# Performance work log

Measured on AMD Instinct MI355X. Metric: run time of the kernel, lower is better.

The kernel has to match this reference:

```python
import jax, jax.numpy as jnp
import numpy as np

NEG = -1e10

def setup_inputs() -> dict:
    key = jax.random.key(0)
    ks = jax.random.split(key, 7)
    B, Q, K = 8, 128, 512
    d_q, d_kv, d_attn = 512, 512, 256
    query = jax.random.normal(ks[0], (B, Q, d_q), dtype=jnp.float32)
    kv = jax.random.normal(ks[1], (B, K, d_kv), dtype=jnp.float32)
    query_len = jax.random.randint(ks[2], (B,), 1, Q + 1)
    kv_len = jax.random.randint(ks[3], (B,), 1, K + 1)
    # h2attn: Linear(d_q+d_kv, d_attn) -> weight [d_attn, d_q+d_kv], bias [d_attn]
    W = jax.random.normal(ks[4], (d_attn, d_q + d_kv), dtype=jnp.float32) / np.sqrt(d_q + d_kv)
    b = jnp.zeros((d_attn,), dtype=jnp.float32)
    v = jax.random.normal(ks[5], (d_attn,), dtype=jnp.float32)
    return {"query": query, "kv": kv, "W": W, "b": b, "v": v,
            "query_len": query_len, "kv_len": kv_len}

def reference(query, kv, W, b, v, query_len, kv_len):
    B, Q, d_q = query.shape
    _, K, d_kv = kv.shape
    # Split the concat-linear: W @ [q; kv] == Wq @ q + Wk @ kv (same math, no huge concat)
    Wq, Wk = W[:, :d_q], W[:, d_q:]
    q_proj = jnp.einsum('bqd,ad->bqa', query, Wq)   # [B,Q,d_attn]
    k_proj = jnp.einsum('bkd,ad->bka', kv, Wk)      # [B,K,d_attn]
    e = jnp.tanh(q_proj[:, :, None, :] + k_proj[:, None, :, :] + b)  # [B,Q,K,d_attn]
    score = jnp.einsum('bqka,a->bqk', e, v)          # [B,Q,K]
    mask_q = jnp.arange(Q)[None, :] < query_len[:, None]   # [B,Q]
    mask_k = jnp.arange(K)[None, :] < kv_len[:, None]      # [B,K]
    score = jnp.where(mask_q[:, :, None], score, NEG)
    score = jnp.where(mask_k[:, None, :], score, NEG)
    attn = jax.nn.softmax(score, axis=-1)
    out = jnp.einsum('bqk,bkd->bqd', attn, kv)       # [B,Q,d_kv]
    return out
```

## Files before the change

### kernel.cpp

```cpp
#include <hip/hip_runtime.h>

#define NEGV (-10000000000.0f)

typedef unsigned short u16;
typedef _Float16 __attribute__((ext_vector_type(8))) f16x8;
typedef _Float16 __attribute__((ext_vector_type(4))) f16x4;
typedef __attribute__((ext_vector_type(4))) float f32x4;

__device__ __forceinline__ u16 f2fh(float f) {
  _Float16 h = (_Float16)f;
  return __builtin_bit_cast(u16, h);
}

__device__ __forceinline__ void gload16(const u16* g, u16* l) {
  __builtin_amdgcn_global_load_lds(
      (const __attribute__((address_space(1))) void*)g,
      (__attribute__((address_space(3))) void*)l, 16, 0, 0);
}

__device__ __forceinline__ f16x8 cvt8(float4 x, float4 y) {
  f16x8 o;
  o[0] = (_Float16)x.x; o[1] = (_Float16)x.y;
  o[2] = (_Float16)x.z; o[3] = (_Float16)x.w;
  o[4] = (_Float16)y.x; o[5] = (_Float16)y.y;
  o[6] = (_Float16)y.z; o[7] = (_Float16)y.w;
  return o;
}

__device__ __forceinline__ void mfma_tile(const u16* sA, const u16* sB,
                                          int l, int wr, int wc,
                                          f32x4 (*acc)[2]) {
#pragma unroll
  for (int ks = 0; ks < 2; ks++) {
    f16x8 af[2], bfr[2];
#pragma unroll
    for (int f = 0; f < 2; f++) {
      int cb = (ks * 32 + ((l >> 4) << 3)) << 1;
      int row = wr * 32 + f * 16 + (l & 15);
      af[f] = *(const f16x8*)((const char*)sA + row * 128 + (cb ^ ((row & 7) << 4)));
      int col = wc * 32 + f * 16 + (l & 15);
      bfr[f] = *(const f16x8*)((const char*)sB + col * 128 + (cb ^ ((col & 7) << 4)));
    }
#pragma unroll
    for (int fm = 0; fm < 2; fm++)
#pragma unroll
      for (int fn = 0; fn < 2; fn++)
        acc[fm][fn] = __builtin_amdgcn_mfma_f32_16x16x32_f16(
            af[fm], bfr[fn], acc[fm][fn], 0, 0, 0);
  }
}

__global__ __launch_bounds__(256) void proj_mfma(
    const float* __restrict__ query, const float* __restrict__ kv,
    const float* __restrict__ W, const float* __restrict__ bias,
    const int* __restrict__ qlen_p, const int* __restrict__ klen_p,
    float* __restrict__ qpE, float* __restrict__ kpE)
{
  const int p = blockIdx.x;
  const int id = (p & 7) * 40 + (p >> 3);
  const int t = threadIdx.x;

  const float *A, *B; float* C;
  int lda, ldb, ldc, bm, bn;
  const float* bp = nullptr;
  if (id < 64) {
    bm = (id >> 2) * 64; bn = (id & 3) * 64;
    if ((bm & 127) >= qlen_p[bm >> 7]) return;
    A = query; lda = 512; B = W; ldb = 1024;
    C = qpE; ldc = 256;
    bp = bias;
  } else {
    int r = id - 64;
    int b = r >> 5, w5 = r & 31;
    bm = (w5 & 3) * 64; bn = (w5 >> 2) * 64;
    if (bn >= klen_p[b]) return;
    A = W + 512; lda = 1024;
    B = kv + (size_t)b * 512 * 512; ldb = 512;
    C = kpE + (size_t)b * 256 * 512; ldc = 512;
  }

  __shared__ __align__(16) u16 sA[8 * 512];
  __shared__ __align__(16) u16 sB[8 * 512];

  const int l = t & 63, w = t >> 6;
  const int wr = w >> 1, wc = w & 1;
  const int r0 = t >> 3, oc = t & 7;
  const int sw0 = (oc * 16) ^ ((r0 & 7) << 4);

  f32x4 acc[2][2] = {};
  float4 a00, a01, a10, a11, b00, b01, b10, b11;

  auto LOAD = [&](int k0) {
    const float* pa0 = A + (size_t)(bm + r0) * lda + k0 + oc * 8;
    const float* pa1 = pa0 + (size_t)32 * lda;
    a00 = *(const float4*)pa0; a01 = *(const float4*)(pa0 + 4);
    a10 = *(const float4*)pa1; a11 = *(const float4*)(pa1 + 4);
    const float* pb0 = B + (size_t)(bn + r0) * ldb + k0 + oc * 8;
    const float* pb1 = pb0 + (size_t)32 * ldb;
    b00 = *(const float4*)pb0; b01 = *(const float4*)(pb0 + 4);
    b10 = *(const float4*)pb1; b11 = *(const float4*)(pb1 + 4);
  };
  auto WRITE = [&]() {
    *(f16x8*)((char*)sA + r0 * 128 + sw0)        = cvt8(a00, a01);
    *(f16x8*)((char*)sA + (r0 + 32) * 128 + sw0) = cvt8(a10, a11);
    *(f16x8*)((char*)sB + r0 * 128 + sw0)        = cvt8(b00, b01);
    *(f16x8*)((char*)sB + (r0 + 32) * 128 + sw0) = cvt8(b10, b11);
  };

  LOAD(0);
  for (int k0 = 0; k0 < 512; k0 += 64) {
    __syncthreads();
    WRITE();
    if (k0 + 64 < 512) LOAD(k0 + 64);
    __syncthreads();
    mfma_tile(sA, sB, l, wr, wc, acc);
  }

#pragma unroll
  for (int fm = 0; fm < 2; fm++)
#pragma unroll
    for (int fn = 0; fn < 2; fn++) {
      int cn = bn + wc * 32 + fn * 16 + (l & 15);
      float bv = bp ? bp[cn] : 0.0f;
#pragma unroll
      for (int j = 0; j < 4; j++) {
        int rm = bm + wr * 32 + fm * 16 + (l >> 4) * 4 + j;
        C[(size_t)rm * ldc + cn] = __expf((acc[fm][fn][j] + bv) * 2.0f);
      }
    }
}

__global__ __launch_bounds__(512) void score_softmax(
    const float* __restrict__ qpE,
    const float* __restrict__ kpE,
    const float* __restrict__ v,
    const int* __restrict__ qlen_p, const int* __restrict__ klen_p,
    u16* __restrict__ P)
{
  const int p = blockIdx.x;
  const int log = (p & 7) * 32 + (p >> 3);
  const int b = log >> 5, q0 = (log & 31) * 4;
  const int t = threadIdx.x;
  const int qlen = qlen_p[b], klen = klen_p[b];
  const int w = t >> 6, l = t & 63;
  const int k = t;
  u16* Pb = P + (size_t)(b * 128 + q0) * 512;

  if (q0 >= qlen) {
    const u16 uh = f2fh(1.0f / 512.0f);
#pragma unroll
    for (int r = 0; r < 4; r++) Pb[(size_t)r * 512 + k] = uh;
    return;
  }

  __shared__ float sEq[256][4];
  __shared__ float sV2[256];
  __shared__ float sRed[8][8];

  {
    int a = t & 255, rr = t >> 8;
    sEq[a][rr]     = qpE[(size_t)(b * 128 + q0 + rr) * 256 + a];
    sEq[a][rr + 2] = qpE[(size_t)(b * 128 + q0 + rr + 2) * 256 + a];
    if (t < 256) sV2[t] = 2.0f * v[t];
  }
  __syncthreads();

  float s[4] = {0.f, 0.f, 0.f, 0.f};
  if (w * 64 < klen) {
    const float* kc = kpE + (size_t)b * 256 * 512 + k;
#pragma unroll 8
    for (int a = 0; a < 256; a++) {
      float ek = kc[(size_t)a * 512];
      f32x4 eq = *(const f32x4*)&sEq[a][0];
      float vv = sV2[a];
#pragma unroll
      for (int r = 0; r < 4; r++)
        s[r] = fmaf(-vv, __builtin_amdgcn_rcpf(fmaf(eq[r], ek, 1.0f)), s[r]);
    }
  }
  if (k >= klen) {
#pragma unroll
    for (int r = 0; r < 4; r++) s[r] = NEGV;
  }

#pragma unroll
  for (int r = 0; r < 4; r++) {
    float x = s[r];
#pragma unroll
    for (int off = 32; off > 0; off >>= 1) x = fmaxf(x, __shfl_xor(x, off));
    if (l == 0) sRed[w][r] = x;
  }
  __syncthreads();
  float e[4];
#pragma unroll
  for (int r = 0; r < 4; r++) {
    float mm = fmaxf(fmaxf(sRed[0][r], sRed[1][r]),
                     fmaxf(sRed[2][r], sRed[3][r]));
    mm = fmaxf(mm, fmaxf(fmaxf(sRed[4][r], sRed[5][r]),
                         fmaxf(sRed[6][r], sRed[7][r])));
    e[r] = __expf(s[r] - mm);
  }
  __syncthreads();
#pragma unroll
  for (int r = 0; r < 4; r++) {
    float x = e[r];
#pragma unroll
    for (int off = 32; off > 0; off >>= 1) x += __shfl_xor(x, off);
    if (l == 0) sRed[w][4 + r] = x;
  }
  __syncthreads();

  const u16 uh = f2fh(1.0f / 512.0f);
#pragma unroll
  for (int r = 0; r < 4; r++) {
    float S = (sRed[0][4 + r] + sRed[1][4 + r]) +
              (sRed[2][4 + r] + sRed[3][4 + r]) +
              (sRed[4][4 + r] + sRed[5][4 + r]) +
              (sRed[6][4 + r] + sRed[7][4 + r]);
    float pp = e[r] * __fdividef(1.0f, S);
    Pb[(size_t)r * 512 + k] = (q0 + r < qlen) ? f2fh(pp) : uh;
  }
}

__global__ __launch_bounds__(256) void pv_mfma(
    const u16* __restrict__ P, const float* __restrict__ kv,
    float* __restrict__ out)
{
  __shared__ __align__(16) u16 sA[8 * 512];
  __shared__ __align__(16) u16 sB[8 * 512];
  const int p = blockIdx.x;
  const int log = (p & 7) * 16 + (p >> 3);
  const int t = threadIdx.x;
  const int b = log >> 4, r = log & 15;
  const int bm = (r >> 3) * 64, bn = (r & 7) * 64;

  const u16* Ab = P + (size_t)b * 128 * 512;
  const float* Bb = kv + (size_t)b * 512 * 512;

  const int l = t & 63, w = t >> 6;
  const int wr = w >> 1, wc = w & 1;
  const int srow = l >> 3, scol = ((l & 7) ^ srow) << 3;

  const int dq = t & 15, kq = t >> 4;

  float4 v0, v1, v2, v3;
  auto LOADB = [&](int k0) {
    const float* pp = Bb + (size_t)(k0 + kq * 4) * 512 + bn + dq * 4;
    v0 = *(const float4*)pp;
    v1 = *(const float4*)(pp + 512);
    v2 = *(const float4*)(pp + 1024);
    v3 = *(const float4*)(pp + 1536);
  };
  auto WRITEB = [&]() {
#define WRB(jj, ee)                                                       \
    { int d = dq * 4 + jj;                                                \
      f16x4 c; c[0] = (_Float16)v0.ee; c[1] = (_Float16)v1.ee;            \
      c[2] = (_Float16)v2.ee; c[3] = (_Float16)v3.ee;                     \
      *(f16x4*)((char*)sB + d * 128 +                                     \
                ((((kq >> 1) * 16) ^ ((d & 7) << 4)) + (kq & 1) * 8)) = c; }
    WRB(0, x) WRB(1, y) WRB(2, z) WRB(3, w)
#undef WRB
  };

  f32x4 acc[2][2] = {};
  LOADB(0);
  for (int k0 = 0; k0 < 512; k0 += 64) {
    __syncthreads();
    WRITEB();
#pragma unroll
    for (int i = 0; i < 2; i++) {
      int s = w * 2 + i;
      gload16(Ab + (size_t)(bm + s * 8 + srow) * 512 + k0 + scol, sA + s * 512);
    }
    if (k0 + 64 < 512) LOADB(k0 + 64);
    __syncthreads();
    mfma_tile(sA, sB, l, wr, wc, acc);
  }

  float* Cb = out + (size_t)b * 128 * 512;
#pragma unroll
  for (int fm = 0; fm < 2; fm++)
#pragma unroll
    for (int fn = 0; fn < 2; fn++) {
      int cn = bn + wc * 32 + fn * 16 + (l & 15);
#pragma unroll
      for (int j = 0; j < 4; j++) {
        int rm = bm + wr * 32 + fm * 16 + (l >> 4) * 4 + j;
        Cb[(size_t)rm * 512 + cn] = acc[fm][fn][j];
      }
    }
}

extern "C" void kernel_launch(void* const* d_in, const int* in_sizes, int n_in,
                              void* d_out, int out_size, void* d_ws, size_t ws_size,
                              hipStream_t stream)
{
  const float* query = (const float*)d_in[0];
  const float* kv    = (const float*)d_in[1];
  const float* W     = (const float*)d_in[2];
  const float* bbias = (const float*)d_in[3];
  const float* v     = (const float*)d_in[4];
  const int*   qlen  = (const int*)d_in[5];
  const int*   klen  = (const int*)d_in[6];
  float* out = (float*)d_out;

  float* qpE = (float*)d_ws;
  float* kpE = qpE + 1024 * 256;
  u16*   P   = (u16*)(kpE + 8 * 256 * 512);

  proj_mfma<<<dim3(320), 256, 0, stream>>>(
      query, kv, W, bbias, qlen, klen, qpE, kpE);

  score_softmax<<<dim3(256), 512, 0, stream>>>(
      qpE, kpE, v, qlen, klen, P);

  pv_mfma<<<dim3(128), 256, 0, stream>>>(P, kv, out);
}
```

Baseline: 40.40 us.

## Use 128x128 tiles for key projection and skip masked K blocks in PV

The key-projection part of proj_mfma now uses 128x128 output tiles with 4x4 MFMA fragments per wave, which cuts the block count from 320 to 128 and increases operand reuse per block. The query projection keeps its 64x64 tiles. In pv_mfma, row blocks whose query rows are all valid loop only up to the padded kv_len, since softmax probabilities past kv_len are zero. The trade-off is fewer, heavier blocks with more registers in the projection, and possibly poorer load balance.

```diff
diff --git a/kernel.cpp b/kernel.cpp
--- a/kernel.cpp
+++ b/kernel.cpp
@@ -50,84 +50,152 @@
   }
 }
 
+__device__ __forceinline__ void mfma_tile128(const u16* sA, const u16* sB,
+                                             int l, int wr, int wc,
+                                             f32x4 (*acc)[4]) {
+#pragma unroll
+  for (int ks = 0; ks < 2; ks++) {
+    f16x8 af[4], bfr[4];
+#pragma unroll
+    for (int f = 0; f < 4; f++) {
+      int cb = (ks * 32 + ((l >> 4) << 3)) << 1;
+      int row = wr * 64 + f * 16 + (l & 15);
+      af[f] = *(const f16x8*)((const char*)sA + row * 128 + (cb ^ ((row & 7) << 4)));
+      int col = wc * 64 + f * 16 + (l & 15);
+      bfr[f] = *(const f16x8*)((const char*)sB + col * 128 + (cb ^ ((col & 7) << 4)));
+    }
+#pragma unroll
+    for (int fm = 0; fm < 4; fm++)
+#pragma unroll
+      for (int fn = 0; fn < 4; fn++)
+        acc[fm][fn] = __builtin_amdgcn_mfma_f32_16x16x32_f16(
+            af[fm], bfr[fn], acc[fm][fn], 0, 0, 0);
+  }
+}
+
 __global__ __launch_bounds__(256) void proj_mfma(
     const float* __restrict__ query, const float* __restrict__ kv,
     const float* __restrict__ W, const float* __restrict__ bias,
     const int* __restrict__ qlen_p, const int* __restrict__ klen_p,
     float* __restrict__ qpE, float* __restrict__ kpE)
 {
+  __shared__ __align__(16) u16 smem[2 * 128 * 64];
+  u16* sA = smem;
+  u16* sB = smem + 128 * 64;
+
   const int p = blockIdx.x;
-  const int id = (p & 7) * 40 + (p >> 3);
+  const int id = (p & 7) * 16 + (p >> 3);
   const int t = threadIdx.x;
-
-  const float *A, *B; float* C;
-  int lda, ldb, ldc, bm, bn;
-  const float* bp = nullptr;
-  if (id < 64) {
-    bm = (id >> 2) * 64; bn = (id & 3) * 64;
-    if ((bm & 127) >= qlen_p[bm >> 7]) return;
-    A = query; lda = 512; B = W; ldb = 1024;
-    C = qpE; ldc = 256;
-    bp = bias;
-  } else {
-    int r = id - 64;
-    int b = r >> 5, w5 = r & 31;
-    bm = (w5 & 3) * 64; bn = (w5 >> 2) * 64;
-    if (bn >= klen_p[b]) return;
-    A = W + 512; lda = 1024;
-    B = kv + (size_t)b * 512 * 512; ldb = 512;
-    C = kpE + (size_t)b * 256 * 512; ldc = 512;
-  }
-
-  __shared__ __align__(16) u16 sA[8 * 512];
-  __shared__ __align__(16) u16 sB[8 * 512];
-
   const int l = t & 63, w = t >> 6;
   const int wr = w >> 1, wc = w & 1;
-  const int r0 = t >> 3, oc = t & 7;
-  const int sw0 = (oc * 16) ^ ((r0 & 7) << 4);
-
-  f32x4 acc[2][2] = {};
-  float4 a00, a01, a10, a11, b00, b01, b10, b11;
-
-  auto LOAD = [&](int k0) {
-    const float* pa0 = A + (size_t)(bm + r0) * lda + k0 + oc * 8;
-    const float* pa1 = pa0 + (size_t)32 * lda;
-    a00 = *(const float4*)pa0; a01 = *(const float4*)(pa0 + 4);
-    a10 = *(const float4*)pa1; a11 = *(const float4*)(pa1 + 4);
-    const float* pb0 = B + (size_t)(bn + r0) * ldb + k0 + oc * 8;
-    const float* pb1 = pb0 + (size_t)32 * ldb;
-    b00 = *(const float4*)pb0; b01 = *(const float4*)(pb0 + 4);
-    b10 = *(const float4*)pb1; b11 = *(const float4*)(pb1 + 4);
-  };
-  auto WRITE = [&]() {
-    *(f16x8*)((char*)sA + r0 * 128 + sw0)        = cvt8(a00, a01);
-    *(f16x8*)((char*)sA + (r0 + 32) * 128 + sw0) = cvt8(a10, a11);
-    *(f16x8*)((char*)sB + r0 * 128 + sw0)        = cvt8(b00, b01);
-    *(f16x8*)((char*)sB + (r0 + 32) * 128 + sw0) = cvt8(b10, b11);
-  };
-
-  LOAD(0);
-  for (int k0 = 0; k0 < 512; k0 += 64) {
-    __syncthreads();
-    WRITE();
-    if (k0 + 64 < 512) LOAD(k0 + 64);
-    __syncthreads();
-    mfma_tile(sA, sB, l, wr, wc, acc);
-  }
-
-#pragma unroll
-  for (int fm = 0; fm < 2; fm++)
-#pragma unroll
-    for (int fn = 0; fn < 2; fn++) {
-      int cn = bn + wc * 32 + fn * 16 + (l & 15);
-      float bv = bp ? bp[cn] : 0.0f;
-#pragma unroll
-      for (int j = 0; j < 4; j++) {
-        int rm = bm + wr * 32 + fm * 16 + (l >> 4) * 4 + j;
-        C[(size_t)rm * ldc + cn] = __expf((acc[fm][fn][j] + bv) * 2.0f);
-      }
-    }
+
+  if (id < 64) {
+    const int bm = (id >> 2) * 64, bn = (id & 3) * 64;
+    if ((bm & 127) >= qlen_p[bm >> 7]) return;
+
+    const float* A = query;
+    const float* B = W;
+    float* C = qpE;
+
+    const int r0 = t >> 3, oc = t & 7;
+    const int sw0 = (oc * 16) ^ ((r0 & 7) << 4);
+
+    f32x4 acc[2][2] = {};
+    float4 a00, a01, a10, a11, b00, b01, b10, b11;
+
+    auto LOAD = [&](int k0) {
+      const float* pa0 = A + (size_t)(bm + r0) * 512 + k0 + oc * 8;
+      const float* pa1 = pa0 + (size_t)32 * 512;
+      a00 = *(const float4*)pa0; a01 = *(const float4*)(pa0 + 4);
+      a10 = *(const float4*)pa1; a11 = *(const float4*)(pa1 + 4);
+      const float* pb0 = B + (size_t)(bn + r0) * 1024 + k0 + oc * 8;
+      const float* pb1 = pb0 + (size_t)32 * 1024;
+      b00 = *(const float4*)pb0; b01 = *(const float4*)(pb0 + 4);
+      b10 = *(const float4*)pb1; b11 = *(const float4*)(pb1 + 4);
+    };
+    auto WRITE = [&]() {
+      *(f16x8*)((char*)sA + r0 * 128 + sw0)        = cvt8(a00, a01);
+      *(f16x8*)((char*)sA + (r0 + 32) * 128 + sw0) = cvt8(a10, a11);
+      *(f16x8*)((char*)sB + r0 * 128 + sw0)        = cvt8(b00, b01);
+      *(f16x8*)((char*)sB + (r0 + 32) * 128 + sw0) = cvt8(b10, b11);
+    };
+
+    LOAD(0);
+    for (int k0 = 0; k0 < 512; k0 += 64) {
+      __syncthreads();
+      WRITE();
+      if (k0 + 64 < 512) LOAD(k0 + 64);
+      __syncthreads();
+      mfma_tile(sA, sB, l, wr, wc, acc);
+    }
+
+#pragma unroll
+    for (int fm = 0; fm < 2; fm++)
+#pragma unroll
+      for (int fn = 0; fn < 2; fn++) {
+        int cn = bn + wc * 32 + fn * 16 + (l & 15);
+        float bv = bias[cn];
+#pragma unroll
+        for (int j = 0; j < 4; j++) {
+          int rm = bm + wr * 32 + fm * 16 + (l >> 4) * 4 + j;
+          C[(size_t)rm * 256 + cn] = __expf((acc[fm][fn][j] + bv) * 2.0f);
+        }
+      }
+  } else {
+    const int r = id - 64;
+    const int b = r >> 3, w5 = r & 7;
+    const int bm = (w5 & 1) * 128;
+    const int bn = (w5 >> 1) * 128;
+    if (bn >= klen_p[b]) return;
+
+    const float* A = W + 512;
+    const float* B = kv + (size_t)b * 512 * 512;
+    float* C = kpE + (size_t)b * 256 * 512;
+
+    const int r0 = t >> 3, oc = t & 7;
+    const int sw0 = (oc * 16) ^ ((r0 & 7) << 4);
+
+    f32x4 acc[4][4] = {};
+    float4 av[4][2], bv[4][2];
+
+    auto LOAD = [&](int k0) {
+#pragma unroll
+      for (int i = 0; i < 4; i++) {
+        const float* pa = A + (size_t)(bm + r0 + 32 * i) * 1024 + k0 + oc * 8;
+        av[i][0] = *(const float4*)pa; av[i][1] = *(const float4*)(pa + 4);
+        const float* pb = B + (size_t)(bn + r0 + 32 * i) * 512 + k0 + oc * 8;
+        bv[i][0] = *(const float4*)pb; bv[i][1] = *(const float4*)(pb + 4);
+      }
+    };
+    auto WRITE = [&]() {
+#pragma unroll
+      for (int i = 0; i < 4; i++) {
+        *(f16x8*)((char*)sA + (r0 + 32 * i) * 128 + sw0) = cvt8(av[i][0], av[i][1]);
+        *(f16x8*)((char*)sB + (r0 + 32 * i) * 128 + sw0) = cvt8(bv[i][0], bv[i][1]);
+      }
+    };
+
+    LOAD(0);
+    for (int k0 = 0; k0 < 512; k0 += 64) {
+      __syncthreads();
+      WRITE();
+      if (k0 + 64 < 512) LOAD(k0 + 64);
+      __syncthreads();
+      mfma_tile128(sA, sB, l, wr, wc, acc);
+    }
+
+#pragma unroll
+    for (int fm = 0; fm < 4; fm++)
+#pragma unroll
+      for (int fn = 0; fn < 4; fn++) {
+        int cn = bn + wc * 64 + fn * 16 + (l & 15);
+#pragma unroll
+        for (int j = 0; j < 4; j++) {
+          int rm = bm + wr * 64 + fm * 16 + (l >> 4) * 4 + j;
+          C[(size_t)rm * 512 + cn] = __expf(acc[fm][fn][j] * 2.0f);
+        }
+      }
+  }
 }
 
 __global__ __launch_bounds__(512) void score_softmax(
@@ -224,6 +292,7 @@
 
 __global__ __launch_bounds__(256) void pv_mfma(
     const u16* __restrict__ P, const float* __restrict__ kv,
+    const int* __restrict__ qlen_p, const int* __restrict__ klen_p,
     float* __restrict__ out)
 {
   __shared__ __align__(16) u16 sA[8 * 512];
@@ -233,6 +302,9 @@
   const int t = threadIdx.x;
   const int b = log >> 4, r = log & 15;
   const int bm = (r >> 3) * 64, bn = (r & 7) * 64;
+
+  const int qlen = qlen_p[b], klen = klen_p[b];
+  const int nk = (bm + 64 <= qlen) ? ((klen + 63) & ~63) : 512;
 
   const u16* Ab = P + (size_t)b * 128 * 512;
   const float* Bb = kv + (size_t)b * 512 * 512;
@@ -264,7 +336,7 @@
 
   f32x4 acc[2][2] = {};
   LOADB(0);
-  for (int k0 = 0; k0 < 512; k0 += 64) {
+  for (int k0 = 0; k0 < nk; k0 += 64) {
     __syncthreads();
     WRITEB();
 #pragma unroll
@@ -272,7 +344,7 @@
       int s = w * 2 + i;
       gload16(Ab + (size_t)(bm + s * 8 + srow) * 512 + k0 + scol, sA + s * 512);
     }
-    if (k0 + 64 < 512) LOADB(k0 + 64);
+    if (k0 + 64 < nk) LOADB(k0 + 64);
     __syncthreads();
     mfma_tile(sA, sB, l, wr, wc, acc);
   }
@@ -308,11 +380,11 @@
   float* kpE = qpE + 1024 * 256;
   u16*   P   = (u16*)(kpE + 8 * 256 * 512);
 
-  proj_mfma<<<dim3(320), 256, 0, stream>>>(
+  proj_mfma<<<dim3(128), 256, 0, stream>>>(
       query, kv, W, bbias, qlen, klen, qpE, kpE);
 
   score_softmax<<<dim3(256), 512, 0, stream>>>(
       qpE, kpE, v, qlen, klen, P);
 
-  pv_mfma<<<dim3(128), 256, 0, stream>>>(P, kv, out);
-}
+  pv_mfma<<<dim3(128), 256, 0, stream>>>(P, kv, qlen, klen, out);
+}
```

Result: slower. 44.84 us (+11.0%).
